# Optimization experiments

Measured on AMD Instinct MI355X. Metric: run time of the kernel, lower is better.

The kernel has to match this reference:

```python
import jax, jax.numpy as jnp
import numpy as np

NEG = -1000000.0  # same finite mask value as the Triton kernel


def setup_inputs() -> dict:
    key = jax.random.key(0)
    k1, k2, k3, k4 = jax.random.split(key, 4)
    B, H, KVH, S, D = 1, 32, 8, 2048, 128
    return {
        "q": jax.random.normal(k1, (B, H, S, D), dtype=jnp.float32),
        "k": jax.random.normal(k2, (B, KVH, S, D), dtype=jnp.float32),
        "v": jax.random.normal(k3, (B, KVH, S, D), dtype=jnp.float32),
        "sinks": jax.random.normal(k4, (H,), dtype=jnp.float32),
        "bandwidth": 1024,
    }


def reference(q, k, v, sinks, bandwidth):
    """Prefill flash attention with causal + sliding-window masking, GQA, and
    per-head attention sinks (extra logit in the softmax denominator)."""
    B, H, S, D = q.shape
    ratio = H // k.shape[1]  # KV_HEAD_RATIO
    kf = jnp.repeat(k, ratio, axis=1)  # [B,H,S,D]
    vf = jnp.repeat(v, ratio, axis=1)
    sm_scale = 1.0 / np.sqrt(D).astype(np.float32)

    logits = jnp.einsum("bhqd,bhkd->bhqk", q, kf) * sm_scale  # [B,H,S,S]
    q_pos = jnp.arange(S)[:, None]
    k_pos = jnp.arange(S)[None, :]
    mask = k_pos > q_pos  # causal
    if bandwidth > 0:
        mask = mask | (k_pos < q_pos - bandwidth + 1)  # sliding window
    logits = jnp.where(mask, NEG, logits)

    sink = sinks[None, :, None]  # [1,H,1] broadcast over batch, query
    m = jnp.maximum(jnp.max(logits, axis=-1), sink)  # [B,H,S]
    p = jnp.exp(logits - m[..., None])
    denom = p.sum(axis=-1) + jnp.exp(sink - m)  # sink contributes to denom only
    out = jnp.einsum("bhqk,bhkd->bhqd", p, vf) / denom[..., None]
    return out
```

## Files before the change

### kernel.cpp

```cpp
#include <hip/hip_runtime.h>
#include <hip/hip_bf16.h>

typedef __bf16 bf16x8 __attribute__((ext_vector_type(8)));
typedef unsigned short u16x8 __attribute__((ext_vector_type(8)));
typedef unsigned int u32x4 __attribute__((ext_vector_type(4)));
typedef float f32x4 __attribute__((ext_vector_type(4)));

#define SLEN 2048
#define DDIM 128
#define NH   32
#define NKVH 8
#define KVB  32
#define MINIT  -1e30f
#define MASKED -3e30f

static __device__ __forceinline__ unsigned short f2bfu(float f) {
  union { float f; unsigned u; } x; x.f = f;
  return (unsigned short)((x.u + 0x7fffu + ((x.u >> 16) & 1u)) >> 16);
}
static __device__ __forceinline__ float bfu2f(unsigned short u) {
  union { unsigned u; float f; } x; x.u = ((unsigned)u) << 16;
  return x.f;
}
static __device__ __forceinline__ unsigned cvt_pk_bf16(float lo, float hi) {
  unsigned r;
  asm("v_cvt_pk_bf16_f32 %0, %1, %2" : "=v"(r) : "v"(lo), "v"(hi));
  return r;
}
static __device__ __forceinline__ f32x4 mfma_bf16(u16x8 a, u16x8 b, f32x4 c) {
  return __builtin_amdgcn_mfma_f32_16x16x32_bf16(
      __builtin_bit_cast(bf16x8, a), __builtin_bit_cast(bf16x8, b), c, 0, 0, 0);
}
static __device__ __forceinline__ int vswz_k(int row) {
  return (row & 3) | (((row >> 3) & 1) << 2);
}

__global__ __launch_bounds__(256) void conv_kv(const float* __restrict__ k,
                                               const float* __restrict__ v,
                                               unsigned* __restrict__ kdst,
                                               unsigned short* __restrict__ vt) {
  __shared__ unsigned T32[32][17];
  const int bb = blockIdx.x;
  if (bb < 1024) {
    const int i = bb * 256 + threadIdx.x;
    const float4 f0 = ((const float4*)k)[2 * i];
    const float4 f1 = ((const float4*)k)[2 * i + 1];
    u32x4 o = { cvt_pk_bf16(f0.x, f0.y), cvt_pk_bf16(f0.z, f0.w),
                cvt_pk_bf16(f1.x, f1.y), cvt_pk_bf16(f1.z, f1.w) };
    ((u32x4*)kdst)[i] = o;
    return;
  }
  const int b   = bb - 1024;
  const int dt  = b & 3;
  const int st  = (b >> 2) & 63;
  const int kvh = b >> 8;
  const int r  = threadIdx.x >> 3;
  const int cg = threadIdx.x & 7;
  const float4 f = *(const float4*)(v + ((size_t)(kvh * SLEN + st * 32 + r) * DDIM) + dt * 32 + cg * 4);
  T32[r][cg * 2]     = cvt_pk_bf16(f.x, f.y);
  T32[r][cg * 2 + 1] = cvt_pk_bf16(f.z, f.w);
  __syncthreads();
  const int dr = threadIdx.x >> 3;
  const unsigned sel = (dr & 1) ? 0x07060302u : 0x05040100u;
  const unsigned a0 = T32[cg * 4 + 0][dr >> 1], a1 = T32[cg * 4 + 1][dr >> 1];
  const unsigned a2 = T32[cg * 4 + 2][dr >> 1], a3 = T32[cg * 4 + 3][dr >> 1];
  unsigned short* vp = vt + (size_t)kvh * DDIM * SLEN + (size_t)(dt * 32 + dr) * SLEN + st * 32 + cg * 4;
  const unsigned w0 = __builtin_amdgcn_perm(a1, a0, sel);
  const unsigned w1 = __builtin_amdgcn_perm(a3, a2, sel);
  vp[0] = (unsigned short)(w0 & 0xffff);
  vp[1] = (unsigned short)(w0 >> 16);
  vp[2] = (unsigned short)(w1 & 0xffff);
  vp[3] = (unsigned short)(w1 >> 16);
}

template <int NCH>
__global__ __launch_bounds__(256, 4) void attn_fwd(
    const float* __restrict__ q, const unsigned short* __restrict__ kbf,
    const unsigned short* __restrict__ vtg, const float* __restrict__ sinks,
    const int* __restrict__ bwp, float* __restrict__ out,
    unsigned short* __restrict__ pO, float* __restrict__ pm,
    float* __restrict__ pl) {
  constexpr int NQT = 32;
  __shared__ unsigned short Kl[KVB * DDIM];
  __shared__ unsigned short Vt[DDIM * KVB];
  __shared__ float SmS[4][16];

  const int tid  = threadIdx.x;
  const int wid  = tid >> 6;
  const int lane = tid & 63;
  const int ln   = lane & 15;
  const int hi   = lane >> 4;

  const int B   = blockIdx.x;
  const int x   = B & 7;
  const int j   = B >> 3;
  constexpr int per = 4 * NCH;
  const int qt  = NQT - 1 - (j / per);
  const int rem = j % per;
  const int hh  = rem / NCH;
  const int c   = rem % NCH;
  const int h   = x * 4 + hh;
  const int kvh = x;
  const int q0  = qt * 64;
  const int qrow0 = q0 + wid * 16;
  const int qpos  = qrow0 + ln;

  const int bwv    = bwp[0];
  const int lo_off = (bwv > 0) ? (bwv - 1) : SLEN;

  const int T0 = max(0, q0 - lo_off) >> 5;
  const int T1 = (q0 + 63) >> 5;
  const int N  = T1 - T0 + 1;
  const int ch = (N + NCH - 1) / NCH;
  const int Ts = T0 + c * ch;
  const int Te = min(T1, Ts + ch - 1);

  const float sm_scale = 0.08838834764831845f;

  u16x8 qf[4];
  {
    const float* qp = q + ((size_t)(h * SLEN + qpos) * DDIM) + hi * 8;
    #pragma unroll
    for (int dk = 0; dk < 4; ++dk) {
      float4 f0 = *(const float4*)(qp + dk * 32);
      float4 f1 = *(const float4*)(qp + dk * 32 + 4);
      u32x4 t = { cvt_pk_bf16(f0.x, f0.y), cvt_pk_bf16(f0.z, f0.w),
                  cvt_pk_bf16(f1.x, f1.y), cvt_pk_bf16(f1.z, f1.w) };
      qf[dk] = __builtin_bit_cast(u16x8, t);
    }
  }

  float m_ln = MINIT, l_ln = 0.0f;
  f32x4 oacc[8];
  #pragma unroll
  for (int nt = 0; nt < 8; ++nt) oacc[nt] = f32x4{0.f, 0.f, 0.f, 0.f};

  const unsigned short* Kg = kbf + (size_t)kvh * SLEN * DDIM;
  const unsigned short* Vg = vtg + (size_t)kvh * DDIM * SLEN;

  const int kr0 = tid >> 4, sk = tid & 15;
  const int kr1 = kr0 + 16;
  const int kw0 = kr0 * DDIM + (((sk & 8) | ((sk & 7) ^ vswz_k(kr0))) * 8);
  const int kw1 = kr1 * DDIM + (((sk & 8) | ((sk & 7) ^ vswz_k(kr1))) * 8);
  const int vr0 = tid >> 2, sv = tid & 3;
  const int vr1 = vr0 + 64;
  const int vw0 = vr0 * KVB + ((sv ^ ((vr0 >> 1) & 3)) * 8);
  const int vw1 = vr1 * KVB + ((sv ^ ((vr1 >> 1) & 3)) * 8);

  const int prow = ((ln >> 2) << 3) | (ln & 3);
  const int vk   = (ln & 3) | (((ln >> 2) & 1) << 2);
  int kfo[4];
  #pragma unroll
  for (int dk = 0; dk < 4; ++dk) {
    const int s = dk * 4 + hi;
    kfo[dk] = prow * DDIM + (((s & 8) | ((s & 7) ^ vk)) * 8);
  }
  const int vro = ln * KVB + ((hi ^ ((ln >> 1) & 3)) * 8);

  if (Ts <= Te) {
    const int kbS = Ts * 32, kbE = Te * 32;

    u16x8 pk0, pk1, pv0, pv1;
    {
      pk0 = *(const u16x8*)(Kg + (size_t)(kbS + kr0) * DDIM + sk * 8);
      pk1 = *(const u16x8*)(Kg + (size_t)(kbS + kr1) * DDIM + sk * 8);
      pv0 = *(const u16x8*)(Vg + (size_t)vr0 * SLEN + kbS + sv * 8);
      pv1 = *(const u16x8*)(Vg + (size_t)vr1 * SLEN + kbS + sv * 8);
    }

    for (int kb = kbS; kb <= kbE; kb += KVB) {
      __syncthreads();
      *(u16x8*)&Kl[kw0] = pk0;
      *(u16x8*)&Kl[kw1] = pk1;
      *(u16x8*)&Vt[vw0] = pv0;
      *(u16x8*)&Vt[vw1] = pv1;
      __syncthreads();

      {
        const int nb = min(kb + KVB, kbE);
        pk0 = *(const u16x8*)(Kg + (size_t)(nb + kr0) * DDIM + sk * 8);
        pk1 = *(const u16x8*)(Kg + (size_t)(nb + kr1) * DDIM + sk * 8);
        pv0 = *(const u16x8*)(Vg + (size_t)vr0 * SLEN + nb + sv * 8);
        pv1 = *(const u16x8*)(Vg + (size_t)vr1 * SLEN + nb + sv * 8);
      }

      if (kb > qrow0 + 15) continue;
      if (kb + KVB - 1 < qrow0 - lo_off) continue;

      f32x4 sacc0 = {0,0,0,0}, sacc1 = {0,0,0,0};
      #pragma unroll
      for (int dk = 0; dk < 4; ++dk) {
        sacc0 = mfma_bf16(*(const u16x8*)&Kl[kfo[dk]], qf[dk], sacc0);
        sacc1 = mfma_bf16(*(const u16x8*)&Kl[kfo[dk] + 4 * DDIM], qf[dk], sacc1);
      }

      float p[8];
      #pragma unroll
      for (int r = 0; r < 4; ++r) {
        const int kp0 = kb + hi * 8 + r;
        const int kp1 = kp0 + 4;
        p[r]     = ((kp0 <= qpos) && (kp0 >= qpos - lo_off)) ? sacc0[r] * sm_scale : MASKED;
        p[4 + r] = ((kp1 <= qpos) && (kp1 >= qpos - lo_off)) ? sacc1[r] * sm_scale : MASKED;
      }

      float mx = fmaxf(fmaxf(fmaxf(p[0], p[1]), fmaxf(p[2], p[3])),
                       fmaxf(fmaxf(p[4], p[5]), fmaxf(p[6], p[7])));
      mx = fmaxf(mx, __shfl_xor(mx, 16));
      mx = fmaxf(mx, __shfl_xor(mx, 32));

      if (__any(mx > m_ln + 8.0f)) {
        const float mn   = fmaxf(m_ln, mx);
        const float corr = __expf(m_ln - mn);
        l_ln *= corr;
        m_ln = mn;
        if (hi == 0) SmS[wid][ln] = corr;
        float c4[4];
        #pragma unroll
        for (int r = 0; r < 4; ++r) c4[r] = SmS[wid][hi * 4 + r];
        #pragma unroll
        for (int nt = 0; nt < 8; ++nt)
          #pragma unroll
          for (int r = 0; r < 4; ++r) oacc[nt][r] *= c4[r];
      }

      float s = 0.0f;
      #pragma unroll
      for (int jj = 0; jj < 8; ++jj) { p[jj] = __expf(p[jj] - m_ln); s += p[jj]; }
      s += __shfl_xor(s, 16);
      s += __shfl_xor(s, 32);
      l_ln += s;

      const u32x4 paw = { cvt_pk_bf16(p[0], p[1]), cvt_pk_bf16(p[2], p[3]),
                          cvt_pk_bf16(p[4], p[5]), cvt_pk_bf16(p[6], p[7]) };
      const u16x8 pa = __builtin_bit_cast(u16x8, paw);

      #pragma unroll
      for (int nt = 0; nt < 8; ++nt) {
        const u16x8 vb = *(const u16x8*)&Vt[vro + nt * 16 * KVB];
        oacc[nt] = mfma_bf16(pa, vb, oacc[nt]);
      }
    }
  }

  if (NCH == 1) {
    const float sink = sinks[h];
    const float M  = fmaxf(m_ln, sink);
    const float ed = __expf(m_ln - M);
    const float fac_ln = ed / (l_ln * ed + __expf(sink - M));
    if (hi == 0) SmS[wid][ln] = fac_ln;
    float fac4[4];
    #pragma unroll
    for (int r = 0; r < 4; ++r) fac4[r] = SmS[wid][hi * 4 + r];
    #pragma unroll
    for (int r = 0; r < 4; ++r) {
      float* op = out + ((size_t)(h * SLEN + qrow0 + hi*4 + r) * DDIM) + ln;
      #pragma unroll
      for (int nt = 0; nt < 8; ++nt) op[nt * 16] = oacc[nt][r] * fac4[r];
    }
  } else {
    const size_t Lb = ((size_t)(h * NQT + qt)) * NCH + c;
    if (hi == 0) {
      pm[Lb * 64 + wid * 16 + ln] = m_ln;
      pl[Lb * 64 + wid * 16 + ln] = l_ln;
    }
    #pragma unroll
    for (int r = 0; r < 4; ++r) {
      unsigned short* po = pO + (Lb * 64 + wid * 16 + hi * 4 + r) * 128 + ln;
      #pragma unroll
      for (int nt = 0; nt < 8; ++nt) po[nt * 16] = f2bfu(oacc[nt][r]);
    }
  }
}

template <int NCH, int QBLK, int NQT>
__global__ __launch_bounds__(256) void mergeN(
    const unsigned short* __restrict__ pO, const float* __restrict__ pm,
    const float* __restrict__ pl, const float* __restrict__ sinks,
    float* __restrict__ out) {
  const int t    = blockIdx.x * 256 + threadIdx.x;
  const int rid  = t >> 2;
  const int d0   = (t & 3) * 32;
  const int h    = rid >> 11;
  const int qpos = rid & 2047;
  const int qt   = qpos / QBLK;
  const int lr   = qpos % QBLK;
  const size_t base = ((size_t)(h * NQT + qt) * NCH) * QBLK + lr;
  const float sink = sinks[h];
  float mc[NCH], lc[NCH];
  float M = sink;
  #pragma unroll
  for (int c = 0; c < NCH; ++c) {
    mc[c] = pm[base + (size_t)c * QBLK];
    lc[c] = pl[base + (size_t)c * QBLK];
    M = fmaxf(M, mc[c]);
  }
  float denom = __expf(sink - M);
  float sc[NCH];
  #pragma unroll
  for (int c = 0; c < NCH; ++c) { sc[c] = __expf(mc[c] - M); denom += lc[c] * sc[c]; }
  const float inv = 1.0f / denom;
  float o[32];
  #pragma unroll
  for (int i = 0; i < 32; ++i) o[i] = 0.f;
  #pragma unroll
  for (int c = 0; c < NCH; ++c) {
    const unsigned short* pp = pO + (base + (size_t)c * QBLK) * 128 + d0;
    const float s = sc[c] * inv;
    #pragma unroll
    for (int i = 0; i < 4; ++i) {
      u16x8 a = *(const u16x8*)(pp + i * 8);
      #pragma unroll
      for (int jj = 0; jj < 8; ++jj) o[i*8+jj] += bfu2f(a[jj]) * s;
    }
  }
  float* op = out + (size_t)rid * 128 + d0;
  #pragma unroll
  for (int i = 0; i < 8; ++i)
    *(float4*)(op + i*4) = make_float4(o[i*4], o[i*4+1], o[i*4+2], o[i*4+3]);
}

extern "C" void kernel_launch(void* const* d_in, const int* in_sizes, int n_in,
                              void* d_out, int out_size, void* d_ws, size_t ws_size,
                              hipStream_t stream) {
  const float* q     = (const float*)d_in[0];
  const float* k     = (const float*)d_in[1];
  const float* v     = (const float*)d_in[2];
  const float* sinks = (const float*)d_in[3];
  const int*   bw    = (const int*)d_in[4];
  float* out = (float*)d_out;

  const size_t kvElems = (size_t)NKVH * SLEN * DDIM;
  unsigned short* kbf = (unsigned short*)d_ws;
  unsigned short* vtg = kbf + kvElems;
  unsigned short* pO  = vtg + kvElems;

  const size_t nPart2 = (size_t)NH * 32 * 2 * 64;
  const size_t need2  = 4 * kvElems + nPart2 * 128 * 2 + nPart2 * 8;

  conv_kv<<<dim3(1024 + NKVH * 64 * 4), 256, 0, stream>>>(k, v, (unsigned*)kbf, vtg);

  if (ws_size >= need2) {
    float* pm = (float*)(pO + nPart2 * 128);
    float* pl = pm + nPart2;
    attn_fwd<2><<<dim3(2048), 256, 0, stream>>>(q, kbf, vtg, sinks, bw, out, pO, pm, pl);
    mergeN<2, 64, 32><<<dim3(1024), 256, 0, stream>>>(pO, pm, pl, sinks, out);
  } else {
    attn_fwd<1><<<dim3(1024), 256, 0, stream>>>(q, kbf, vtg, sinks, bw, out, pO, nullptr, nullptr);
  }
}
```

Baseline: 75.27 us.

## Double query rows per wave to reuse K/V tiles, use exp2 softmax

Each wave now handles 32 query rows (two 16-row groups) instead of 16, so the query block grows from 64 to 128 and every K/V tile loaded into LDS feeds twice as many MFMAs. Softmax switches to base-2 exponentials with the scale folded into log2e, and interior tiles skip the per-element mask check. The cost is higher register pressure (occupancy hint lowered from 4 to 3) and half as many blocks, which may hurt load balance across CUs.

```diff
diff --git a/kernel.cpp b/kernel.cpp
--- a/kernel.cpp
+++ b/kernel.cpp
@@ -13,6 +13,7 @@
 #define KVB  32
 #define MINIT  -1e30f
 #define MASKED -3e30f
+#define LOG2E  1.4426950408889634f
 
 static __device__ __forceinline__ unsigned short f2bfu(float f) {
   union { float f; unsigned u; } x; x.f = f;
@@ -74,16 +75,17 @@
 }
 
 template <int NCH>
-__global__ __launch_bounds__(256, 4) void attn_fwd(
+__global__ __launch_bounds__(256, 3) void attn_fwd(
     const float* __restrict__ q, const unsigned short* __restrict__ kbf,
     const unsigned short* __restrict__ vtg, const float* __restrict__ sinks,
     const int* __restrict__ bwp, float* __restrict__ out,
     unsigned short* __restrict__ pO, float* __restrict__ pm,
     float* __restrict__ pl) {
-  constexpr int NQT = 32;
+  constexpr int QBLK = 128;
+  constexpr int NQT  = SLEN / QBLK;
   __shared__ unsigned short Kl[KVB * DDIM];
   __shared__ unsigned short Vt[DDIM * KVB];
-  __shared__ float SmS[4][16];
+  __shared__ float SmS[4][2][16];
 
   const int tid  = threadIdx.x;
   const int wid  = tid >> 6;
@@ -101,39 +103,41 @@
   const int c   = rem % NCH;
   const int h   = x * 4 + hh;
   const int kvh = x;
-  const int q0  = qt * 64;
-  const int qrow0 = q0 + wid * 16;
-  const int qpos  = qrow0 + ln;
+  const int q0  = qt * QBLK;
+  const int qrow0 = q0 + wid * 32;
 
   const int bwv    = bwp[0];
   const int lo_off = (bwv > 0) ? (bwv - 1) : SLEN;
 
   const int T0 = max(0, q0 - lo_off) >> 5;
-  const int T1 = (q0 + 63) >> 5;
+  const int T1 = (q0 + QBLK - 1) >> 5;
   const int N  = T1 - T0 + 1;
   const int ch = (N + NCH - 1) / NCH;
   const int Ts = T0 + c * ch;
   const int Te = min(T1, Ts + ch - 1);
 
-  const float sm_scale = 0.08838834764831845f;
-
-  u16x8 qf[4];
-  {
-    const float* qp = q + ((size_t)(h * SLEN + qpos) * DDIM) + hi * 8;
+  const float c2 = 0.08838834764831845f * LOG2E;
+
+  u16x8 qf[2][4];
+  #pragma unroll
+  for (int g = 0; g < 2; ++g) {
+    const float* qp = q + ((size_t)(h * SLEN + qrow0 + g * 16 + ln) * DDIM) + hi * 8;
     #pragma unroll
     for (int dk = 0; dk < 4; ++dk) {
       float4 f0 = *(const float4*)(qp + dk * 32);
       float4 f1 = *(const float4*)(qp + dk * 32 + 4);
       u32x4 t = { cvt_pk_bf16(f0.x, f0.y), cvt_pk_bf16(f0.z, f0.w),
                   cvt_pk_bf16(f1.x, f1.y), cvt_pk_bf16(f1.z, f1.w) };
-      qf[dk] = __builtin_bit_cast(u16x8, t);
-    }
-  }
-
-  float m_ln = MINIT, l_ln = 0.0f;
-  f32x4 oacc[8];
-  #pragma unroll
-  for (int nt = 0; nt < 8; ++nt) oacc[nt] = f32x4{0.f, 0.f, 0.f, 0.f};
+      qf[g][dk] = __builtin_bit_cast(u16x8, t);
+    }
+  }
+
+  float m2[2] = {MINIT, MINIT}, l[2] = {0.0f, 0.0f};
+  f32x4 oacc[2][8];
+  #pragma unroll
+  for (int g = 0; g < 2; ++g)
+    #pragma unroll
+    for (int nt = 0; nt < 8; ++nt) oacc[g][nt] = f32x4{0.f, 0.f, 0.f, 0.f};
 
   const unsigned short* Kg = kbf + (size_t)kvh * SLEN * DDIM;
   const unsigned short* Vg = vtg + (size_t)kvh * DDIM * SLEN;
@@ -184,90 +188,139 @@
         pv1 = *(const u16x8*)(Vg + (size_t)vr1 * SLEN + nb + sv * 8);
       }
 
-      if (kb > qrow0 + 15) continue;
+      if (kb > qrow0 + 31) continue;
       if (kb + KVB - 1 < qrow0 - lo_off) continue;
 
-      f32x4 sacc0 = {0,0,0,0}, sacc1 = {0,0,0,0};
+      f32x4 sacc[2][2];
+      #pragma unroll
+      for (int g = 0; g < 2; ++g) { sacc[g][0] = f32x4{0,0,0,0}; sacc[g][1] = f32x4{0,0,0,0}; }
       #pragma unroll
       for (int dk = 0; dk < 4; ++dk) {
-        sacc0 = mfma_bf16(*(const u16x8*)&Kl[kfo[dk]], qf[dk], sacc0);
-        sacc1 = mfma_bf16(*(const u16x8*)&Kl[kfo[dk] + 4 * DDIM], qf[dk], sacc1);
-      }
-
-      float p[8];
-      #pragma unroll
-      for (int r = 0; r < 4; ++r) {
-        const int kp0 = kb + hi * 8 + r;
-        const int kp1 = kp0 + 4;
-        p[r]     = ((kp0 <= qpos) && (kp0 >= qpos - lo_off)) ? sacc0[r] * sm_scale : MASKED;
-        p[4 + r] = ((kp1 <= qpos) && (kp1 >= qpos - lo_off)) ? sacc1[r] * sm_scale : MASKED;
-      }
-
-      float mx = fmaxf(fmaxf(fmaxf(p[0], p[1]), fmaxf(p[2], p[3])),
-                       fmaxf(fmaxf(p[4], p[5]), fmaxf(p[6], p[7])));
-      mx = fmaxf(mx, __shfl_xor(mx, 16));
-      mx = fmaxf(mx, __shfl_xor(mx, 32));
-
-      if (__any(mx > m_ln + 8.0f)) {
-        const float mn   = fmaxf(m_ln, mx);
-        const float corr = __expf(m_ln - mn);
-        l_ln *= corr;
-        m_ln = mn;
-        if (hi == 0) SmS[wid][ln] = corr;
-        float c4[4];
-        #pragma unroll
-        for (int r = 0; r < 4; ++r) c4[r] = SmS[wid][hi * 4 + r];
-        #pragma unroll
-        for (int nt = 0; nt < 8; ++nt)
+        const u16x8 kf0 = *(const u16x8*)&Kl[kfo[dk]];
+        const u16x8 kf1 = *(const u16x8*)&Kl[kfo[dk] + 4 * DDIM];
+        sacc[0][0] = mfma_bf16(kf0, qf[0][dk], sacc[0][0]);
+        sacc[1][0] = mfma_bf16(kf0, qf[1][dk], sacc[1][0]);
+        sacc[0][1] = mfma_bf16(kf1, qf[0][dk], sacc[0][1]);
+        sacc[1][1] = mfma_bf16(kf1, qf[1][dk], sacc[1][1]);
+      }
+
+      float p[2][8];
+      const bool interior = (kb + KVB - 1 <= qrow0) && (kb >= qrow0 + 31 - lo_off);
+      if (interior) {
+        #pragma unroll
+        for (int g = 0; g < 2; ++g)
           #pragma unroll
-          for (int r = 0; r < 4; ++r) oacc[nt][r] *= c4[r];
-      }
-
-      float s = 0.0f;
-      #pragma unroll
-      for (int jj = 0; jj < 8; ++jj) { p[jj] = __expf(p[jj] - m_ln); s += p[jj]; }
-      s += __shfl_xor(s, 16);
-      s += __shfl_xor(s, 32);
-      l_ln += s;
-
-      const u32x4 paw = { cvt_pk_bf16(p[0], p[1]), cvt_pk_bf16(p[2], p[3]),
-                          cvt_pk_bf16(p[4], p[5]), cvt_pk_bf16(p[6], p[7]) };
-      const u16x8 pa = __builtin_bit_cast(u16x8, paw);
+          for (int r = 0; r < 4; ++r) {
+            p[g][r]     = sacc[g][0][r] * c2;
+            p[g][4 + r] = sacc[g][1][r] * c2;
+          }
+      } else {
+        #pragma unroll
+        for (int g = 0; g < 2; ++g) {
+          const int qpos = qrow0 + g * 16 + ln;
+          #pragma unroll
+          for (int r = 0; r < 4; ++r) {
+            const int kp0 = kb + hi * 8 + r;
+            const int kp1 = kp0 + 4;
+            p[g][r]     = ((kp0 <= qpos) && (kp0 >= qpos - lo_off)) ? sacc[g][0][r] * c2 : MASKED;
+            p[g][4 + r] = ((kp1 <= qpos) && (kp1 >= qpos - lo_off)) ? sacc[g][1][r] * c2 : MASKED;
+          }
+        }
+      }
+
+      float mx[2];
+      bool need = false;
+      #pragma unroll
+      for (int g = 0; g < 2; ++g) {
+        float t = fmaxf(fmaxf(fmaxf(p[g][0], p[g][1]), fmaxf(p[g][2], p[g][3])),
+                        fmaxf(fmaxf(p[g][4], p[g][5]), fmaxf(p[g][6], p[g][7])));
+        t = fmaxf(t, __shfl_xor(t, 16));
+        t = fmaxf(t, __shfl_xor(t, 32));
+        mx[g] = t;
+        need = need || (t > m2[g] + 11.5415605f);
+      }
+
+      if (__any(need)) {
+        #pragma unroll
+        for (int g = 0; g < 2; ++g) {
+          const float mn   = fmaxf(m2[g], mx[g]);
+          const float corr = exp2f(m2[g] - mn);
+          l[g] *= corr;
+          m2[g] = mn;
+          if (hi == 0) SmS[wid][g][ln] = corr;
+        }
+        #pragma unroll
+        for (int g = 0; g < 2; ++g) {
+          float c4[4];
+          #pragma unroll
+          for (int r = 0; r < 4; ++r) c4[r] = SmS[wid][g][hi * 4 + r];
+          #pragma unroll
+          for (int nt = 0; nt < 8; ++nt)
+            #pragma unroll
+            for (int r = 0; r < 4; ++r) oacc[g][nt][r] *= c4[r];
+        }
+      }
+
+      #pragma unroll
+      for (int g = 0; g < 2; ++g) {
+        float s = 0.0f;
+        #pragma unroll
+        for (int jj = 0; jj < 8; ++jj) { p[g][jj] = exp2f(p[g][jj] - m2[g]); s += p[g][jj]; }
+        s += __shfl_xor(s, 16);
+        s += __shfl_xor(s, 32);
+        l[g] += s;
+      }
+
+      u16x8 pa[2];
+      #pragma unroll
+      for (int g = 0; g < 2; ++g) {
+        const u32x4 paw = { cvt_pk_bf16(p[g][0], p[g][1]), cvt_pk_bf16(p[g][2], p[g][3]),
+                            cvt_pk_bf16(p[g][4], p[g][5]), cvt_pk_bf16(p[g][6], p[g][7]) };
+        pa[g] = __builtin_bit_cast(u16x8, paw);
+      }
 
       #pragma unroll
       for (int nt = 0; nt < 8; ++nt) {
         const u16x8 vb = *(const u16x8*)&Vt[vro + nt * 16 * KVB];
-        oacc[nt] = mfma_bf16(pa, vb, oacc[nt]);
+        oacc[0][nt] = mfma_bf16(pa[0], vb, oacc[0][nt]);
+        oacc[1][nt] = mfma_bf16(pa[1], vb, oacc[1][nt]);
       }
     }
   }
 
   if (NCH == 1) {
-    const float sink = sinks[h];
-    const float M  = fmaxf(m_ln, sink);
-    const float ed = __expf(m_ln - M);
-    const float fac_ln = ed / (l_ln * ed + __expf(sink - M));
-    if (hi == 0) SmS[wid][ln] = fac_ln;
-    float fac4[4];
+    const float sk2 = sinks[h] * LOG2E;
     #pragma unroll
-    for (int r = 0; r < 4; ++r) fac4[r] = SmS[wid][hi * 4 + r];
-    #pragma unroll
-    for (int r = 0; r < 4; ++r) {
-      float* op = out + ((size_t)(h * SLEN + qrow0 + hi*4 + r) * DDIM) + ln;
-      #pragma unroll
-      for (int nt = 0; nt < 8; ++nt) op[nt * 16] = oacc[nt][r] * fac4[r];
+    for (int g = 0; g < 2; ++g) {
+      const float M  = fmaxf(m2[g], sk2);
+      const float ed = exp2f(m2[g] - M);
+      const float fac_ln = ed / (l[g] * ed + exp2f(sk2 - M));
+      if (hi == 0) SmS[wid][g][ln] = fac_ln;
+      float fac4[4];
+      #pragma unroll
+      for (int r = 0; r < 4; ++r) fac4[r] = SmS[wid][g][hi * 4 + r];
+      #pragma unroll
+      for (int r = 0; r < 4; ++r) {
+        float* op = out + ((size_t)(h * SLEN + qrow0 + g*16 + hi*4 + r) * DDIM) + ln;
+        #pragma unroll
+        for (int nt = 0; nt < 8; ++nt) op[nt * 16] = oacc[g][nt][r] * fac4[r];
+      }
     }
   } else {
     const size_t Lb = ((size_t)(h * NQT + qt)) * NCH + c;
-    if (hi == 0) {
-      pm[Lb * 64 + wid * 16 + ln] = m_ln;
-      pl[Lb * 64 + wid * 16 + ln] = l_ln;
-    }
     #pragma unroll
-    for (int r = 0; r < 4; ++r) {
-      unsigned short* po = pO + (Lb * 64 + wid * 16 + hi * 4 + r) * 128 + ln;
-      #pragma unroll
-      for (int nt = 0; nt < 8; ++nt) po[nt * 16] = f2bfu(oacc[nt][r]);
+    for (int g = 0; g < 2; ++g) {
+      const int rbase = wid * 32 + g * 16;
+      if (hi == 0) {
+        pm[Lb * QBLK + rbase + ln] = m2[g];
+        pl[Lb * QBLK + rbase + ln] = l[g];
+      }
+      #pragma unroll
+      for (int r = 0; r < 4; ++r) {
+        unsigned short* po = pO + (Lb * QBLK + rbase + hi * 4 + r) * 128 + ln;
+        #pragma unroll
+        for (int nt = 0; nt < 8; ++nt) po[nt * 16] = f2bfu(oacc[g][nt][r]);
+      }
     }
   }
 }
@@ -285,19 +338,19 @@
   const int qt   = qpos / QBLK;
   const int lr   = qpos % QBLK;
   const size_t base = ((size_t)(h * NQT + qt) * NCH) * QBLK + lr;
-  const float sink = sinks[h];
+  const float sk2 = sinks[h] * LOG2E;
   float mc[NCH], lc[NCH];
-  float M = sink;
+  float M = sk2;
   #pragma unroll
   for (int c = 0; c < NCH; ++c) {
     mc[c] = pm[base + (size_t)c * QBLK];
     lc[c] = pl[base + (size_t)c * QBLK];
     M = fmaxf(M, mc[c]);
   }
-  float denom = __expf(sink - M);
+  float denom = exp2f(sk2 - M);
   float sc[NCH];
   #pragma unroll
-  for (int c = 0; c < NCH; ++c) { sc[c] = __expf(mc[c] - M); denom += lc[c] * sc[c]; }
+  for (int c = 0; c < NCH; ++c) { sc[c] = exp2f(mc[c] - M); denom += lc[c] * sc[c]; }
   const float inv = 1.0f / denom;
   float o[32];
   #pragma unroll
@@ -334,7 +387,7 @@
   unsigned short* vtg = kbf + kvElems;
   unsigned short* pO  = vtg + kvElems;
 
-  const size_t nPart2 = (size_t)NH * 32 * 2 * 64;
+  const size_t nPart2 = (size_t)NH * 16 * 2 * 128;
   const size_t need2  = 4 * kvElems + nPart2 * 128 * 2 + nPart2 * 8;
 
   conv_kv<<<dim3(1024 + NKVH * 64 * 4), 256, 0, stream>>>(k, v, (unsigned*)kbf, vtg);
@@ -342,9 +395,9 @@
   if (ws_size >= need2) {
     float* pm = (float*)(pO + nPart2 * 128);
     float* pl = pm + nPart2;
-    attn_fwd<2><<<dim3(2048), 256, 0, stream>>>(q, kbf, vtg, sinks, bw, out, pO, pm, pl);
-    mergeN<2, 64, 32><<<dim3(1024), 256, 0, stream>>>(pO, pm, pl, sinks, out);
+    attn_fwd<2><<<dim3(1024), 256, 0, stream>>>(q, kbf, vtg, sinks, bw, out, pO, pm, pl);
+    mergeN<2, 128, 16><<<dim3(1024), 256, 0, stream>>>(pO, pm, pl, sinks, out);
   } else {
-    attn_fwd<1><<<dim3(1024), 256, 0, stream>>>(q, kbf, vtg, sinks, bw, out, pO, nullptr, nullptr);
-  }
-}
+    attn_fwd<1><<<dim3(512), 256, 0, stream>>>(q, kbf, vtg, sinks, bw, out, pO, nullptr, nullptr);
+  }
+}
```

Measured after the change: 90.50 us. 1.2x slower.

## Double-buffer K/V LDS tiles, use exp2 softmax, and skip masking on interior tiles

Applied to the files above, without the earlier changes.

Splits the K and V shared-memory tiles into two buffers so each iteration writes the next tile while computing on the current one, which removes one __syncthreads per iteration. The softmax moves to base-2 by folding log2(e) into the scale, the sink and the merge kernel, and the lazy-rescale threshold is adjusted to match. Tiles that sit fully inside the causal and sliding window skip the per-element mask compare. s_setprio is raised around the MFMA blocks. In exchange the kernel uses twice the LDS per block, which may reduce occupancy.

```diff
diff --git a/kernel.cpp b/kernel.cpp
--- a/kernel.cpp
+++ b/kernel.cpp
@@ -13,6 +13,7 @@
 #define KVB  32
 #define MINIT  -1e30f
 #define MASKED -3e30f
+#define LOG2E  1.4426950408889634f
 
 static __device__ __forceinline__ unsigned short f2bfu(float f) {
   union { float f; unsigned u; } x; x.f = f;
@@ -81,8 +82,8 @@
     unsigned short* __restrict__ pO, float* __restrict__ pm,
     float* __restrict__ pl) {
   constexpr int NQT = 32;
-  __shared__ unsigned short Kl[KVB * DDIM];
-  __shared__ unsigned short Vt[DDIM * KVB];
+  __shared__ unsigned short Kl[2][KVB * DDIM];
+  __shared__ unsigned short Vt[2][DDIM * KVB];
   __shared__ float SmS[4][16];
 
   const int tid  = threadIdx.x;
@@ -115,7 +116,7 @@
   const int Ts = T0 + c * ch;
   const int Te = min(T1, Ts + ch - 1);
 
-  const float sm_scale = 0.08838834764831845f;
+  const float c2 = 0.08838834764831845f * LOG2E;
 
   u16x8 qf[4];
   {
@@ -130,7 +131,7 @@
     }
   }
 
-  float m_ln = MINIT, l_ln = 0.0f;
+  float m2 = MINIT, l_ln = 0.0f;
   f32x4 oacc[8];
   #pragma unroll
   for (int nt = 0; nt < 8; ++nt) oacc[nt] = f32x4{0.f, 0.f, 0.f, 0.f};
@@ -161,92 +162,118 @@
     const int kbS = Ts * 32, kbE = Te * 32;
 
     u16x8 pk0, pk1, pv0, pv1;
+    pk0 = *(const u16x8*)(Kg + (size_t)(kbS + kr0) * DDIM + sk * 8);
+    pk1 = *(const u16x8*)(Kg + (size_t)(kbS + kr1) * DDIM + sk * 8);
+    pv0 = *(const u16x8*)(Vg + (size_t)vr0 * SLEN + kbS + sv * 8);
+    pv1 = *(const u16x8*)(Vg + (size_t)vr1 * SLEN + kbS + sv * 8);
+    *(u16x8*)&Kl[0][kw0] = pk0;
+    *(u16x8*)&Kl[0][kw1] = pk1;
+    *(u16x8*)&Vt[0][vw0] = pv0;
+    *(u16x8*)&Vt[0][vw1] = pv1;
     {
-      pk0 = *(const u16x8*)(Kg + (size_t)(kbS + kr0) * DDIM + sk * 8);
-      pk1 = *(const u16x8*)(Kg + (size_t)(kbS + kr1) * DDIM + sk * 8);
-      pv0 = *(const u16x8*)(Vg + (size_t)vr0 * SLEN + kbS + sv * 8);
-      pv1 = *(const u16x8*)(Vg + (size_t)vr1 * SLEN + kbS + sv * 8);
-    }
-
+      const int nb = min(kbS + KVB, kbE);
+      pk0 = *(const u16x8*)(Kg + (size_t)(nb + kr0) * DDIM + sk * 8);
+      pk1 = *(const u16x8*)(Kg + (size_t)(nb + kr1) * DDIM + sk * 8);
+      pv0 = *(const u16x8*)(Vg + (size_t)vr0 * SLEN + nb + sv * 8);
+      pv1 = *(const u16x8*)(Vg + (size_t)vr1 * SLEN + nb + sv * 8);
+    }
+
+    int cur = 0;
     for (int kb = kbS; kb <= kbE; kb += KVB) {
       __syncthreads();
-      *(u16x8*)&Kl[kw0] = pk0;
-      *(u16x8*)&Kl[kw1] = pk1;
-      *(u16x8*)&Vt[vw0] = pv0;
-      *(u16x8*)&Vt[vw1] = pv1;
-      __syncthreads();
-
+      const int nxt = cur ^ 1;
+      *(u16x8*)&Kl[nxt][kw0] = pk0;
+      *(u16x8*)&Kl[nxt][kw1] = pk1;
+      *(u16x8*)&Vt[nxt][vw0] = pv0;
+      *(u16x8*)&Vt[nxt][vw1] = pv1;
       {
-        const int nb = min(kb + KVB, kbE);
+        const int nb = min(kb + 2 * KVB, kbE);
         pk0 = *(const u16x8*)(Kg + (size_t)(nb + kr0) * DDIM + sk * 8);
         pk1 = *(const u16x8*)(Kg + (size_t)(nb + kr1) * DDIM + sk * 8);
         pv0 = *(const u16x8*)(Vg + (size_t)vr0 * SLEN + nb + sv * 8);
         pv1 = *(const u16x8*)(Vg + (size_t)vr1 * SLEN + nb + sv * 8);
       }
 
-      if (kb > qrow0 + 15) continue;
-      if (kb + KVB - 1 < qrow0 - lo_off) continue;
-
-      f32x4 sacc0 = {0,0,0,0}, sacc1 = {0,0,0,0};
-      #pragma unroll
-      for (int dk = 0; dk < 4; ++dk) {
-        sacc0 = mfma_bf16(*(const u16x8*)&Kl[kfo[dk]], qf[dk], sacc0);
-        sacc1 = mfma_bf16(*(const u16x8*)&Kl[kfo[dk] + 4 * DDIM], qf[dk], sacc1);
+      const bool skip = (kb > qrow0 + 15) || (kb + KVB - 1 < qrow0 - lo_off);
+      if (!skip) {
+        const unsigned short* kbp = &Kl[cur][0];
+        const unsigned short* vbp = &Vt[cur][0];
+
+        f32x4 sacc0 = {0,0,0,0}, sacc1 = {0,0,0,0};
+        __builtin_amdgcn_s_setprio(1);
+        #pragma unroll
+        for (int dk = 0; dk < 4; ++dk) {
+          sacc0 = mfma_bf16(*(const u16x8*)(kbp + kfo[dk]), qf[dk], sacc0);
+          sacc1 = mfma_bf16(*(const u16x8*)(kbp + kfo[dk] + 4 * DDIM), qf[dk], sacc1);
+        }
+        __builtin_amdgcn_s_setprio(0);
+
+        float p[8];
+        const bool interior = (kb + KVB - 1 <= qrow0) && (kb >= qrow0 + 15 - lo_off);
+        if (interior) {
+          #pragma unroll
+          for (int r = 0; r < 4; ++r) {
+            p[r]     = sacc0[r] * c2;
+            p[4 + r] = sacc1[r] * c2;
+          }
+        } else {
+          #pragma unroll
+          for (int r = 0; r < 4; ++r) {
+            const int kp0 = kb + hi * 8 + r;
+            const int kp1 = kp0 + 4;
+            p[r]     = ((kp0 <= qpos) && (kp0 >= qpos - lo_off)) ? sacc0[r] * c2 : MASKED;
+            p[4 + r] = ((kp1 <= qpos) && (kp1 >= qpos - lo_off)) ? sacc1[r] * c2 : MASKED;
+          }
+        }
+
+        float mx = fmaxf(fmaxf(fmaxf(p[0], p[1]), fmaxf(p[2], p[3])),
+                         fmaxf(fmaxf(p[4], p[5]), fmaxf(p[6], p[7])));
+        mx = fmaxf(mx, __shfl_xor(mx, 16));
+        mx = fmaxf(mx, __shfl_xor(mx, 32));
+
+        if (__any(mx > m2 + 11.5415605f)) {
+          const float mn   = fmaxf(m2, mx);
+          const float corr = exp2f(m2 - mn);
+          l_ln *= corr;
+          m2 = mn;
+          if (hi == 0) SmS[wid][ln] = corr;
+          float c4[4];
+          #pragma unroll
+          for (int r = 0; r < 4; ++r) c4[r] = SmS[wid][hi * 4 + r];
+          #pragma unroll
+          for (int nt = 0; nt < 8; ++nt)
+            #pragma unroll
+            for (int r = 0; r < 4; ++r) oacc[nt][r] *= c4[r];
+        }
+
+        float s = 0.0f;
+        #pragma unroll
+        for (int jj = 0; jj < 8; ++jj) { p[jj] = exp2f(p[jj] - m2); s += p[jj]; }
+        s += __shfl_xor(s, 16);
+        s += __shfl_xor(s, 32);
+        l_ln += s;
+
+        const u32x4 paw = { cvt_pk_bf16(p[0], p[1]), cvt_pk_bf16(p[2], p[3]),
+                            cvt_pk_bf16(p[4], p[5]), cvt_pk_bf16(p[6], p[7]) };
+        const u16x8 pa = __builtin_bit_cast(u16x8, paw);
+
+        __builtin_amdgcn_s_setprio(1);
+        #pragma unroll
+        for (int nt = 0; nt < 8; ++nt) {
+          const u16x8 vb = *(const u16x8*)(vbp + vro + nt * 16 * KVB);
+          oacc[nt] = mfma_bf16(pa, vb, oacc[nt]);
+        }
+        __builtin_amdgcn_s_setprio(0);
       }
-
-      float p[8];
-      #pragma unroll
-      for (int r = 0; r < 4; ++r) {
-        const int kp0 = kb + hi * 8 + r;
-        const int kp1 = kp0 + 4;
-        p[r]     = ((kp0 <= qpos) && (kp0 >= qpos - lo_off)) ? sacc0[r] * sm_scale : MASKED;
-        p[4 + r] = ((kp1 <= qpos) && (kp1 >= qpos - lo_off)) ? sacc1[r] * sm_scale : MASKED;
-      }
-
-      float mx = fmaxf(fmaxf(fmaxf(p[0], p[1]), fmaxf(p[2], p[3])),
-                       fmaxf(fmaxf(p[4], p[5]), fmaxf(p[6], p[7])));
-      mx = fmaxf(mx, __shfl_xor(mx, 16));
-      mx = fmaxf(mx, __shfl_xor(mx, 32));
-
-      if (__any(mx > m_ln + 8.0f)) {
-        const float mn   = fmaxf(m_ln, mx);
-        const float corr = __expf(m_ln - mn);
-        l_ln *= corr;
-        m_ln = mn;
-        if (hi == 0) SmS[wid][ln] = corr;
-        float c4[4];
-        #pragma unroll
-        for (int r = 0; r < 4; ++r) c4[r] = SmS[wid][hi * 4 + r];
-        #pragma unroll
-        for (int nt = 0; nt < 8; ++nt)
-          #pragma unroll
-          for (int r = 0; r < 4; ++r) oacc[nt][r] *= c4[r];
-      }
-
-      float s = 0.0f;
-      #pragma unroll
-      for (int jj = 0; jj < 8; ++jj) { p[jj] = __expf(p[jj] - m_ln); s += p[jj]; }
-      s += __shfl_xor(s, 16);
-      s += __shfl_xor(s, 32);
-      l_ln += s;
-
-      const u32x4 paw = { cvt_pk_bf16(p[0], p[1]), cvt_pk_bf16(p[2], p[3]),
-                          cvt_pk_bf16(p[4], p[5]), cvt_pk_bf16(p[6], p[7]) };
-      const u16x8 pa = __builtin_bit_cast(u16x8, paw);
-
-      #pragma unroll
-      for (int nt = 0; nt < 8; ++nt) {
-        const u16x8 vb = *(const u16x8*)&Vt[vro + nt * 16 * KVB];
-        oacc[nt] = mfma_bf16(pa, vb, oacc[nt]);
-      }
+      cur ^= 1;
     }
   }
 
   if (NCH == 1) {
-    const float sink = sinks[h];
-    const float M  = fmaxf(m_ln, sink);
-    const float ed = __expf(m_ln - M);
-    const float fac_ln = ed / (l_ln * ed + __expf(sink - M));
+    const float sk2 = sinks[h] * LOG2E;
+    const float M  = fmaxf(m2, sk2);
+    const float ed = exp2f(m2 - M);
+    const float fac_ln = ed / (l_ln * ed + exp2f(sk2 - M));
     if (hi == 0) SmS[wid][ln] = fac_ln;
     float fac4[4];
     #pragma unroll
@@ -260,7 +287,7 @@
   } else {
     const size_t Lb = ((size_t)(h * NQT + qt)) * NCH + c;
     if (hi == 0) {
-      pm[Lb * 64 + wid * 16 + ln] = m_ln;
+      pm[Lb * 64 + wid * 16 + ln] = m2;
       pl[Lb * 64 + wid * 16 + ln] = l_ln;
     }
     #pragma unroll
@@ -285,19 +312,19 @@
   const int qt   = qpos / QBLK;
   const int lr   = qpos % QBLK;
   const size_t base = ((size_t)(h * NQT + qt) * NCH) * QBLK + lr;
-  const float sink = sinks[h];
+  const float sk2 = sinks[h] * LOG2E;
   float mc[NCH], lc[NCH];
-  float M = sink;
+  float M = sk2;
   #pragma unroll
   for (int c = 0; c < NCH; ++c) {
     mc[c] = pm[base + (size_t)c * QBLK];
     lc[c] = pl[base + (size_t)c * QBLK];
     M = fmaxf(M, mc[c]);
   }
-  float denom = __expf(sink - M);
+  float denom = exp2f(sk2 - M);
   float sc[NCH];
   #pragma unroll
-  for (int c = 0; c < NCH; ++c) { sc[c] = __expf(mc[c] - M); denom += lc[c] * sc[c]; }
+  for (int c = 0; c < NCH; ++c) { sc[c] = exp2f(mc[c] - M); denom += lc[c] * sc[c]; }
   const float inv = 1.0f / denom;
   float o[32];
   #pragma unroll
```

Result: slower. 77.75 us (+3.3%).
